# Kernel tuning notes

Hardware: AMD Instinct MI355X
Metric: run time of the kernel (lower is better)

## Reference

```python
import jax, jax.numpy as jnp
import numpy as np

N_NODES = 16384
FM = 256
N_EDGES = 524288


def gcn_conv(x, W, b, edge_index, edge_weight):
    """PyG GCNConv: y = D^-1/2 (A+I) D^-1/2 (x @ W) + b, with edge weights."""
    n = x.shape[0]
    loop = jnp.arange(n)
    src = jnp.concatenate([edge_index[0], loop])
    dst = jnp.concatenate([edge_index[1], loop])
    w = jnp.concatenate([edge_weight, jnp.ones((n,), edge_weight.dtype)])
    deg = jax.ops.segment_sum(w, dst, num_segments=n)
    dinv = jnp.where(deg > 0, jax.lax.rsqrt(jnp.maximum(deg, 1e-30)), 0.0)
    norm = dinv[src] * w * dinv[dst]            # [E+n]
    h = x @ W                                    # [n, fm]
    msg = h[src] * norm[:, None]                 # [E+n, fm] gather
    return jax.ops.segment_sum(msg, dst, num_segments=n) + b


def setup_inputs() -> dict:
    key = jax.random.key(0)
    ks = jax.random.split(key, 24)
    inp = {
        "x": jax.random.normal(ks[0], (N_NODES, FM), jnp.float32),
        "edges_f": jax.random.randint(ks[1], (2, N_EDGES), 0, N_NODES),
        "ew_f": jax.random.uniform(ks[2], (N_EDGES,), jnp.float32),
        "edges_s": jax.random.randint(ks[3], (2, N_EDGES), 0, N_NODES),
        "ew_s": jax.random.uniform(ks[4], (N_EDGES,), jnp.float32),
        "edges_g": jax.random.randint(ks[5], (2, N_EDGES), 0, N_NODES),
        "ew_g": jax.random.uniform(ks[6], (N_EDGES,), jnp.float32),
    }
    names = ["f1", "f2", "s1", "s2", "g1", "g2"]
    for i, nm in enumerate(names):
        inp["W" + nm] = 0.05 * jax.random.normal(ks[7 + i], (FM, FM), jnp.float32)
        inp["b" + nm] = jnp.zeros((FM,), jnp.float32)
    inp["fc1_w"] = 0.5 * jax.random.normal(ks[13], (30, 6), jnp.float32)
    inp["fc1_b"] = jnp.zeros((30,), jnp.float32)
    inp["fc2_w"] = 0.5 * jax.random.normal(ks[14], (6, 30), jnp.float32)
    inp["fc2_b"] = jnp.zeros((6,), jnp.float32)
    inp["cnn_w"] = 0.5 * jax.random.normal(ks[15], (6,), jnp.float32)
    inp["cnn_b"] = jnp.zeros((1,), jnp.float32)
    return inp


def reference(x, edges_f, ew_f, edges_s, ew_s, edges_g, ew_g,
              Wf1, bf1, Wf2, bf2, Ws1, bs1, Ws2, bs2, Wg1, bg1, Wg2, bg2,
              fc1_w, fc1_b, fc2_w, fc2_b, cnn_w, cnn_b):
    # three 2-layer GCN branches with relu
    f1 = jax.nn.relu(gcn_conv(x, Wf1, bf1, edges_f, ew_f))
    f2 = jax.nn.relu(gcn_conv(f1, Wf2, bf2, edges_f, ew_f))
    s1 = jax.nn.relu(gcn_conv(x, Ws1, bs1, edges_s, ew_s))
    s2 = jax.nn.relu(gcn_conv(s1, Ws2, bs2, edges_s, ew_s))
    g1 = jax.nn.relu(gcn_conv(x, Wg1, bg1, edges_g, ew_g))
    g2 = jax.nn.relu(gcn_conv(g1, Wg2, bg2, edges_g, ew_g))
    # cat along features then t().view(1,6,fm,N) == stack of transposed branches
    XM = jnp.stack([f1.T, f2.T, s1.T, s2.T, g1.T, g2.T])  # [6, fm, N]
    # SE channel attention
    pooled = jnp.mean(XM, axis=(1, 2))                     # [6]
    h = jax.nn.relu(fc1_w @ pooled + fc1_b)                # [30]
    att = jax.nn.sigmoid(fc2_w @ h + fc2_b)                # [6]
    XM_att = jax.nn.relu(att[:, None, None] * XM)          # [6, fm, N]
    # 1x1 conv 6->1 channels
    out = jnp.einsum('c,cfn->fn', cnn_w, XM_att) + cnn_b[0]  # [fm, N]
    return out.T                                            # [N, fm]
```

## Files before the change

kernel.cpp:

```cpp
#include <hip/hip_runtime.h>
#include <hip/hip_bf16.h>

#define N_NODES 16384
#define FM      256
#define NF      (N_NODES * FM)
#define NF4     (NF / 4)

typedef __attribute__((ext_vector_type(8))) short short8;
typedef __attribute__((ext_vector_type(4))) float f32x4;

__device__ inline ushort f2bf(float f) {
    uint u = __float_as_uint(f);
    return (ushort)((u + 0x7FFFu + ((u >> 16) & 1u)) >> 16);
}
__device__ inline uint pack2bf(float a, float b) {
    return (uint)f2bf(a) | ((uint)f2bf(b) << 16);
}
__device__ inline float bf2f(ushort u) { return __uint_as_float(((uint)u) << 16); }

__global__ void init_kernel(float* __restrict__ dinv3, int* __restrict__ cnt3,
                            float* __restrict__ pooled) {
    int i = blockIdx.x * blockDim.x + threadIdx.x;
    int n3 = 3 * N_NODES;
    if (i < n3) {
        dinv3[i] = 1.0f;
        cnt3[i] = 0;
    } else if (i < n3 + 6) {
        pooled[i - n3] = 0.0f;
    }
}

__global__ void deg_edges_all(const int* __restrict__ d0, const int* __restrict__ d1,
                              const int* __restrict__ d2,
                              const float* __restrict__ e0, const float* __restrict__ e1,
                              const float* __restrict__ e2,
                              float* __restrict__ deg3, int* __restrict__ cnt3, int E) {
    int t = blockIdx.y;
    const int* dst = (t == 0) ? d0 : (t == 1) ? d1 : d2;
    const float* ew = (t == 0) ? e0 : (t == 1) ? e1 : e2;
    float* deg = deg3 + t * N_NODES;
    int* cnt = cnt3 + t * N_NODES;
    int e = blockIdx.x * blockDim.x + threadIdx.x;
    if (e < E) {
        int d = dst[e];
        atomicAdd(&deg[d], ew[e]);
        atomicAdd(&cnt[d], 1);
    }
}

__global__ void deg_finish_kernel(float* __restrict__ deg, int n3) {
    int i = blockIdx.x * blockDim.x + threadIdx.x;
    if (i < n3) deg[i] = rsqrtf(deg[i]);
}

__global__ __launch_bounds__(1024) void scan_all(const int* __restrict__ cnt3,
                                                 int* __restrict__ rowstart3,
                                                 int* __restrict__ cursor3) {
    const int* cnt = cnt3 + blockIdx.x * N_NODES;
    int* row_start = rowstart3 + blockIdx.x * (N_NODES + 2);
    int* cursor = cursor3 + blockIdx.x * N_NODES;
    __shared__ int part[1024];
    int t = threadIdx.x;
    int base = t * 16;
    int local[16];
    int s = 0;
#pragma unroll
    for (int i = 0; i < 16; ++i) { local[i] = cnt[base + i]; s += local[i]; }
    part[t] = s;
    __syncthreads();
    for (int off = 1; off < 1024; off <<= 1) {
        int v = (t >= off) ? part[t - off] : 0;
        __syncthreads();
        part[t] += v;
        __syncthreads();
    }
    int pre = (t > 0) ? part[t - 1] : 0;
#pragma unroll
    for (int i = 0; i < 16; ++i) {
        row_start[base + i] = pre;
        cursor[base + i] = pre;
        pre += local[i];
    }
    if (t == 1023) row_start[N_NODES] = pre;
}

__global__ void scatter_all(const int* __restrict__ s0, const int* __restrict__ s1,
                            const int* __restrict__ s2,
                            const float* __restrict__ e0, const float* __restrict__ e1,
                            const float* __restrict__ e2,
                            const float* __restrict__ dinv3,
                            int* __restrict__ cursor3,
                            int* __restrict__ csrsrc3, float* __restrict__ csrnorm3,
                            int E) {
    int t = blockIdx.y;
    const int* ed = (t == 0) ? s0 : (t == 1) ? s1 : s2;
    const float* ew = (t == 0) ? e0 : (t == 1) ? e1 : e2;
    const float* dinv = dinv3 + t * N_NODES;
    int* cursor = cursor3 + t * N_NODES;
    int* csr_src = csrsrc3 + (size_t)t * E;
    float* csr_norm = csrnorm3 + (size_t)t * E;
    int e = blockIdx.x * blockDim.x + threadIdx.x;
    if (e >= E) return;
    int s = ed[e], d = ed[E + e];
    int pos = atomicAdd(&cursor[d], 1);
    csr_src[pos] = s;
    csr_norm[pos] = dinv[s] * ew[e] * dinv[d];
}

__global__ __launch_bounds__(256) void wpack_kernel(const float* __restrict__ w0,
                                                    const float* __restrict__ w1,
                                                    const float* __restrict__ w2,
                                                    const float* __restrict__ w3,
                                                    const float* __restrict__ w4,
                                                    const float* __restrict__ w5,
                                                    ushort* __restrict__ wt) {
    const float* W;
    switch (blockIdx.z) {
        case 0: W = w0; break; case 1: W = w1; break; case 2: W = w2; break;
        case 3: W = w3; break; case 4: W = w4; break; default: W = w5; break;
    }
    __shared__ float tl[16][17];
    int tx = threadIdx.x & 15, ty = threadIdx.x >> 4;
    int k0 = blockIdx.x * 16, n0 = blockIdx.y * 16;
    tl[ty][tx] = W[(size_t)(k0 + ty) * FM + n0 + tx];
    __syncthreads();
    wt[(size_t)blockIdx.z * FM * FM + (size_t)(n0 + ty) * FM + k0 + tx] = f2bf(tl[tx][ty]);
}

__global__ __launch_bounds__(256) void gemm_mfma(const float* __restrict__ A,
                                                 const ushort* __restrict__ WT,
                                                 ushort* __restrict__ C) {
    __shared__ ushort A_lds[128 * 64];

    const int tid = threadIdx.x;
    const int lane = tid & 63;
    const int wid = tid >> 6;
    const int wm = wid >> 1, wn = wid & 1;
    const int bm = blockIdx.x * 128;
    const int bn = blockIdx.y * 64;

    const int l15 = lane & 15;
    const int lg = lane >> 4;

    f32x4 acc[4][2];
#pragma unroll
    for (int i = 0; i < 4; ++i)
#pragma unroll
        for (int n = 0; n < 2; ++n) acc[i][n] = (f32x4){0.f, 0.f, 0.f, 0.f};

    const int srow = tid >> 1;
    const int shk = tid & 1;
    const float* arow_p = &A[(size_t)(bm + srow) * FM + shk * 32];

    for (int k0 = 0; k0 < 256; k0 += 64) {
        {
            const float* ap = arow_p + k0;
#pragma unroll
            for (int g = 0; g < 4; ++g) {
                float4 a0 = *(const float4*)(ap + g * 8);
                float4 a1 = *(const float4*)(ap + g * 8 + 4);
                uint4 pk;
                pk.x = pack2bf(a0.x, a0.y);
                pk.y = pack2bf(a0.z, a0.w);
                pk.z = pack2bf(a1.x, a1.y);
                pk.w = pack2bf(a1.z, a1.w);
                int kk = shk * 32 + g * 8;
                int idx = srow * 64 + (kk ^ ((srow & 7) << 3));
                *(uint4*)&A_lds[idx] = pk;
            }
        }
        __syncthreads();
#pragma unroll
        for (int s = 0; s < 2; ++s) {
            short8 bfrag[2];
#pragma unroll
            for (int n = 0; n < 2; ++n) {
                int col = bn + wn * 32 + n * 16 + l15;
                bfrag[n] = *(const short8*)&WT[(size_t)col * FM + k0 + s * 32 + lg * 8];
            }
#pragma unroll
            for (int i = 0; i < 4; ++i) {
                int row = wm * 64 + i * 16 + l15;
                int kk = s * 32 + lg * 8;
                short8 afrag = *(const short8*)&A_lds[row * 64 + (kk ^ ((row & 7) << 3))];
#pragma unroll
                for (int n = 0; n < 2; ++n)
                    acc[i][n] = __builtin_amdgcn_mfma_f32_16x16x32_bf16(
                        afrag, bfrag[n], acc[i][n], 0, 0, 0);
            }
        }
        __syncthreads();
    }
#pragma unroll
    for (int i = 0; i < 4; ++i) {
#pragma unroll
        for (int n = 0; n < 2; ++n) {
            int col = bn + wn * 32 + n * 16 + l15;
#pragma unroll
            for (int r = 0; r < 4; ++r) {
                int row = bm + wm * 64 + i * 16 + lg * 4 + r;
                C[(size_t)row * FM + col] = f2bf(acc[i][n][r]);
            }
        }
    }
}

__global__ __launch_bounds__(256) void gcn_aggregate_csr(const ushort* __restrict__ h,
                                                         const int* __restrict__ row_start,
                                                         const int* __restrict__ csr_src,
                                                         const float* __restrict__ csr_norm,
                                                         const float* __restrict__ dinv,
                                                         const float* __restrict__ bias,
                                                         float* __restrict__ out) {
    int node = blockIdx.x * 4 + (threadIdx.x >> 6);
    int lane = threadIdx.x & 63;
    const ushort4* hp = (const ushort4*)h;

    float di = dinv[node];
    float sw = di * di;
    ushort4 q = hp[(size_t)node * 64 + lane];
    float4 accA = make_float4(bf2f(q.x) * sw, bf2f(q.y) * sw,
                              bf2f(q.z) * sw, bf2f(q.w) * sw);
    float4 accB = make_float4(0.f, 0.f, 0.f, 0.f);

    int beg = row_start[node];
    int end = row_start[node + 1];
    int j = beg;
    for (; j + 3 < end; j += 4) {
        int s0 = csr_src[j];
        int s1 = csr_src[j + 1];
        int s2 = csr_src[j + 2];
        int s3 = csr_src[j + 3];
        float w0 = csr_norm[j];
        float w1 = csr_norm[j + 1];
        float w2 = csr_norm[j + 2];
        float w3 = csr_norm[j + 3];
        ushort4 q0 = hp[(size_t)s0 * 64 + lane];
        ushort4 q1 = hp[(size_t)s1 * 64 + lane];
        ushort4 q2 = hp[(size_t)s2 * 64 + lane];
        ushort4 q3 = hp[(size_t)s3 * 64 + lane];
        accA.x += w0 * bf2f(q0.x) + w1 * bf2f(q1.x);
        accA.y += w0 * bf2f(q0.y) + w1 * bf2f(q1.y);
        accA.z += w0 * bf2f(q0.z) + w1 * bf2f(q1.z);
        accA.w += w0 * bf2f(q0.w) + w1 * bf2f(q1.w);
        accB.x += w2 * bf2f(q2.x) + w3 * bf2f(q3.x);
        accB.y += w2 * bf2f(q2.y) + w3 * bf2f(q3.y);
        accB.z += w2 * bf2f(q2.z) + w3 * bf2f(q3.z);
        accB.w += w2 * bf2f(q2.w) + w3 * bf2f(q3.w);
    }
    for (; j < end; ++j) {
        int s0 = csr_src[j];
        float w0 = csr_norm[j];
        ushort4 q0 = hp[(size_t)s0 * 64 + lane];
        accA.x += w0 * bf2f(q0.x);
        accA.y += w0 * bf2f(q0.y);
        accA.z += w0 * bf2f(q0.z);
        accA.w += w0 * bf2f(q0.w);
    }
    float4 bb = ((const float4*)bias)[lane];
    float4 acc;
    acc.x = fmaxf(accA.x + accB.x + bb.x, 0.0f);
    acc.y = fmaxf(accA.y + accB.y + bb.y, 0.0f);
    acc.z = fmaxf(accA.z + accB.z + bb.z, 0.0f);
    acc.w = fmaxf(accA.w + accB.w + bb.w, 0.0f);
    ((float4*)out)[(size_t)node * 64 + lane] = acc;
}

__global__ __launch_bounds__(256) void reduce_branch_kernel(const float* __restrict__ br,
                                                            float* __restrict__ pooled) {
    int c = blockIdx.y;
    const float4* p = (const float4*)(br + (size_t)c * NF + (size_t)blockIdx.x * 16384);
    float s = 0.0f;
#pragma unroll
    for (int i = 0; i < 16; ++i) {
        float4 v = p[threadIdx.x + i * 256];
        s += v.x + v.y + v.z + v.w;
    }
    for (int o = 32; o > 0; o >>= 1) s += __shfl_down(s, o);
    __shared__ float wsum[4];
    if ((threadIdx.x & 63) == 0) wsum[threadIdx.x >> 6] = s;
    __syncthreads();
    if (threadIdx.x == 0)
        atomicAdd(&pooled[c], wsum[0] + wsum[1] + wsum[2] + wsum[3]);
}

__global__ void se_kernel(const float* __restrict__ pooled_sum,
                          const float* __restrict__ fc1_w, const float* __restrict__ fc1_b,
                          const float* __restrict__ fc2_w, const float* __restrict__ fc2_b,
                          float* __restrict__ att) {
    __shared__ float p[6];
    __shared__ float hbuf[30];
    int t = threadIdx.x;
    if (t < 6) p[t] = pooled_sum[t] * (1.0f / ((float)N_NODES * (float)FM));
    __syncthreads();
    if (t < 30) {
        float a = fc1_b[t];
#pragma unroll
        for (int c = 0; c < 6; ++c) a += fc1_w[t * 6 + c] * p[c];
        hbuf[t] = fmaxf(a, 0.0f);
    }
    __syncthreads();
    if (t < 6) {
        float a = fc2_b[t];
#pragma unroll
        for (int j = 0; j < 30; ++j) a += fc2_w[t * 30 + j] * hbuf[j];
        att[t] = 1.0f / (1.0f + expf(-a));
    }
}

__global__ void combine_kernel(const float* __restrict__ br,
                               const float* __restrict__ att,
                               const float* __restrict__ cnn_w,
                               const float* __restrict__ cnn_b,
                               float* __restrict__ out, int total4) {
    int i = blockIdx.x * blockDim.x + threadIdx.x;
    if (i >= total4) return;
    float a[6], w[6];
#pragma unroll
    for (int c = 0; c < 6; ++c) { a[c] = att[c]; w[c] = cnn_w[c]; }
    float cb = cnn_b[0];
    float4 acc = make_float4(cb, cb, cb, cb);
#pragma unroll
    for (int c = 0; c < 6; ++c) {
        float4 v = ((const float4*)(br + (size_t)c * NF))[i];
        acc.x += w[c] * fmaxf(a[c] * v.x, 0.0f);
        acc.y += w[c] * fmaxf(a[c] * v.y, 0.0f);
        acc.z += w[c] * fmaxf(a[c] * v.z, 0.0f);
        acc.w += w[c] * fmaxf(a[c] * v.w, 0.0f);
    }
    ((float4*)out)[i] = acc;
}


static void run_conv(const float* in, const ushort* wtp, const float* b,
                     const int* row_start, const int* csr_src, const float* csr_norm,
                     const float* dinv, ushort* h_bf16, float* out,
                     hipStream_t stream) {
    dim3 ggrid(N_NODES / 128, FM / 64);
    gemm_mfma<<<ggrid, 256, 0, stream>>>(in, wtp, h_bf16);
    gcn_aggregate_csr<<<N_NODES / 4, 256, 0, stream>>>(h_bf16, row_start, csr_src,
                                                       csr_norm, dinv, b, out);
}

extern "C" void kernel_launch(void* const* d_in, const int* in_sizes, int n_in,
                              void* d_out, int out_size, void* d_ws, size_t ws_size,
                              hipStream_t stream) {
    const float* x      = (const float*)d_in[0];
    const int*   ed_f   = (const int*)d_in[1];
    const float* ew_f   = (const float*)d_in[2];
    const int*   ed_s   = (const int*)d_in[3];
    const float* ew_s   = (const float*)d_in[4];
    const int*   ed_g   = (const int*)d_in[5];
    const float* ew_g   = (const float*)d_in[6];
    const float* Wf1 = (const float*)d_in[7];  const float* bf1 = (const float*)d_in[8];
    const float* Wf2 = (const float*)d_in[9];  const float* bf2 = (const float*)d_in[10];
    const float* Ws1 = (const float*)d_in[11]; const float* bs1 = (const float*)d_in[12];
    const float* Ws2 = (const float*)d_in[13]; const float* bs2 = (const float*)d_in[14];
    const float* Wg1 = (const float*)d_in[15]; const float* bg1 = (const float*)d_in[16];
    const float* Wg2 = (const float*)d_in[17]; const float* bg2 = (const float*)d_in[18];
    const float* fc1_w = (const float*)d_in[19]; const float* fc1_b = (const float*)d_in[20];
    const float* fc2_w = (const float*)d_in[21]; const float* fc2_b = (const float*)d_in[22];
    const float* cnn_w = (const float*)d_in[23]; const float* cnn_b = (const float*)d_in[24];

    const int E = in_sizes[1] / 2;

    float* ws = (float*)d_ws;
    float* br = ws;
    float* dinv3  = ws + (size_t)6 * NF;
    float* pooled = dinv3 + 3 * N_NODES;
    float* att    = pooled + 6;
    int*   cnt3      = (int*)(att + 10);
    int*   cursor3   = cnt3 + 3 * N_NODES;
    int*   rowstart3 = cursor3 + 3 * N_NODES;
    int*   csr_src3  = rowstart3 + 3 * (N_NODES + 2);
    float* csr_norm3 = (float*)(csr_src3 + (size_t)3 * E);
    ushort* wt       = (ushort*)(csr_norm3 + (size_t)3 * E);

    float* dinv_set[3] = { dinv3, dinv3 + N_NODES, dinv3 + 2 * N_NODES };
    int*   rs_set[3]   = { rowstart3, rowstart3 + (N_NODES + 2),
                           rowstart3 + 2 * (N_NODES + 2) };
    int*   csrc_set[3] = { csr_src3, csr_src3 + E, csr_src3 + 2 * E };
    float* cnorm_set[3] = { csr_norm3, csr_norm3 + E, csr_norm3 + 2 * E };

    float* f1 = br + (size_t)0 * NF;
    float* f2 = br + (size_t)1 * NF;
    float* s1 = br + (size_t)2 * NF;
    float* s2 = br + (size_t)3 * NF;
    float* g1 = br + (size_t)4 * NF;
    float* g2 = br + (size_t)5 * NF;

    ushort* h = (ushort*)d_out;

    int n3 = 3 * N_NODES;
    init_kernel<<<(n3 + 6 + 255) / 256, 256, 0, stream>>>(dinv3, cnt3, pooled);
    {
        dim3 dg((E + 255) / 256, 3);
        deg_edges_all<<<dg, 256, 0, stream>>>(ed_f + E, ed_s + E, ed_g + E,
                                              ew_f, ew_s, ew_g, dinv3, cnt3, E);
    }
    deg_finish_kernel<<<(n3 + 255) / 256, 256, 0, stream>>>(dinv3, n3);
    scan_all<<<3, 1024, 0, stream>>>(cnt3, rowstart3, cursor3);
    {
        dim3 sg((E + 255) / 256, 3);
        scatter_all<<<sg, 256, 0, stream>>>(ed_f, ed_s, ed_g, ew_f, ew_s, ew_g,
                                            dinv3, cursor3, csr_src3, csr_norm3, E);
    }
    {
        dim3 wg(16, 16, 6);
        wpack_kernel<<<wg, 256, 0, stream>>>(Wf1, Wf2, Ws1, Ws2, Wg1, Wg2, wt);
    }
    const ushort* wt_set[6] = { wt, wt + 65536, wt + 2 * 65536,
                                wt + 3 * 65536, wt + 4 * 65536, wt + 5 * 65536 };

    run_conv(x,  wt_set[0], bf1, rs_set[0], csrc_set[0], cnorm_set[0], dinv_set[0], h, f1, stream);
    run_conv(f1, wt_set[1], bf2, rs_set[0], csrc_set[0], cnorm_set[0], dinv_set[0], h, f2, stream);
    run_conv(x,  wt_set[2], bs1, rs_set[1], csrc_set[1], cnorm_set[1], dinv_set[1], h, s1, stream);
    run_conv(s1, wt_set[3], bs2, rs_set[1], csrc_set[1], cnorm_set[1], dinv_set[1], h, s2, stream);
    run_conv(x,  wt_set[4], bg1, rs_set[2], csrc_set[2], cnorm_set[2], dinv_set[2], h, g1, stream);
    run_conv(g1, wt_set[5], bg2, rs_set[2], csrc_set[2], cnorm_set[2], dinv_set[2], h, g2, stream);

    dim3 rgrid(256, 6);
    reduce_branch_kernel<<<rgrid, 256, 0, stream>>>(br, pooled);
    se_kernel<<<1, 64, 0, stream>>>(pooled, fc1_w, fc1_b, fc2_w, fc2_b, att);

    combine_kernel<<<NF4 / 256, 256, 0, stream>>>(br, att, cnn_w, cnn_b,
                                                  (float*)d_out, NF4);
}
```

Baseline: 608.5 us.

## Store branch activations in bf16, pack CSR as int2, fuse pooling into aggregation

Branch outputs are now stored as bf16 instead of fp32, which halves the bytes written by aggregation and read by the next GEMM and the combine kernel. x is converted to bf16 once so the GEMM loads bf16 directly. The CSR source index and weight are packed into one int2 array, and degree and norm are computed per row from the CSR instead of with float atomics. The SE mean is accumulated inside the aggregation kernel, which removes the separate reduce pass. The trade-off is extra rounding of intermediate activations and two extra small preprocessing kernels.

```diff
diff --git a/kernel.cpp b/kernel.cpp
--- a/kernel.cpp
+++ b/kernel.cpp
@@ -7,6 +7,7 @@
 #define NF4     (NF / 4)
 
 typedef __attribute__((ext_vector_type(8))) short short8;
+typedef __attribute__((ext_vector_type(8))) ushort ushort8;
 typedef __attribute__((ext_vector_type(4))) float f32x4;
 
 __device__ inline ushort f2bf(float f) {
@@ -18,39 +19,21 @@
 }
 __device__ inline float bf2f(ushort u) { return __uint_as_float(((uint)u) << 16); }
 
-__global__ void init_kernel(float* __restrict__ dinv3, int* __restrict__ cnt3,
-                            float* __restrict__ pooled) {
+__global__ void init_kernel(int* __restrict__ cnt3, float* __restrict__ pooled) {
     int i = blockIdx.x * blockDim.x + threadIdx.x;
     int n3 = 3 * N_NODES;
-    if (i < n3) {
-        dinv3[i] = 1.0f;
-        cnt3[i] = 0;
-    } else if (i < n3 + 6) {
-        pooled[i - n3] = 0.0f;
-    }
-}
-
-__global__ void deg_edges_all(const int* __restrict__ d0, const int* __restrict__ d1,
+    if (i < n3) cnt3[i] = 0;
+    else if (i < n3 + 6) pooled[i - n3] = 0.0f;
+}
+
+__global__ void cnt_edges_all(const int* __restrict__ d0, const int* __restrict__ d1,
                               const int* __restrict__ d2,
-                              const float* __restrict__ e0, const float* __restrict__ e1,
-                              const float* __restrict__ e2,
-                              float* __restrict__ deg3, int* __restrict__ cnt3, int E) {
+                              int* __restrict__ cnt3, int E) {
     int t = blockIdx.y;
     const int* dst = (t == 0) ? d0 : (t == 1) ? d1 : d2;
-    const float* ew = (t == 0) ? e0 : (t == 1) ? e1 : e2;
-    float* deg = deg3 + t * N_NODES;
     int* cnt = cnt3 + t * N_NODES;
     int e = blockIdx.x * blockDim.x + threadIdx.x;
-    if (e < E) {
-        int d = dst[e];
-        atomicAdd(&deg[d], ew[e]);
-        atomicAdd(&cnt[d], 1);
-    }
-}
-
-__global__ void deg_finish_kernel(float* __restrict__ deg, int n3) {
-    int i = blockIdx.x * blockDim.x + threadIdx.x;
-    if (i < n3) deg[i] = rsqrtf(deg[i]);
+    if (e < E) atomicAdd(&cnt[dst[e]], 1);
 }
 
 __global__ __launch_bounds__(1024) void scan_all(const int* __restrict__ cnt3,
@@ -88,23 +71,44 @@
                             const int* __restrict__ s2,
                             const float* __restrict__ e0, const float* __restrict__ e1,
                             const float* __restrict__ e2,
-                            const float* __restrict__ dinv3,
-                            int* __restrict__ cursor3,
-                            int* __restrict__ csrsrc3, float* __restrict__ csrnorm3,
-                            int E) {
+                            int* __restrict__ cursor3, int2* __restrict__ csr3, int E) {
     int t = blockIdx.y;
     const int* ed = (t == 0) ? s0 : (t == 1) ? s1 : s2;
     const float* ew = (t == 0) ? e0 : (t == 1) ? e1 : e2;
-    const float* dinv = dinv3 + t * N_NODES;
     int* cursor = cursor3 + t * N_NODES;
-    int* csr_src = csrsrc3 + (size_t)t * E;
-    float* csr_norm = csrnorm3 + (size_t)t * E;
+    int2* csr = csr3 + (size_t)t * E;
     int e = blockIdx.x * blockDim.x + threadIdx.x;
     if (e >= E) return;
     int s = ed[e], d = ed[E + e];
     int pos = atomicAdd(&cursor[d], 1);
-    csr_src[pos] = s;
-    csr_norm[pos] = dinv[s] * ew[e] * dinv[d];
+    csr[pos] = make_int2(s, __float_as_int(ew[e]));
+}
+
+__global__ __launch_bounds__(256) void deg_dinv_all(const int2* __restrict__ csr3,
+                                                    const int* __restrict__ rowstart3,
+                                                    float* __restrict__ dinv3, int E) {
+    int t = blockIdx.y;
+    const int2* csr = csr3 + (size_t)t * E;
+    const int* row_start = rowstart3 + t * (N_NODES + 2);
+    int node = blockIdx.x * 4 + (threadIdx.x >> 6);
+    int lane = threadIdx.x & 63;
+    int beg = row_start[node], end = row_start[node + 1];
+    float s = 0.0f;
+    for (int j = beg + lane; j < end; j += 64)
+        s += __int_as_float(csr[j].y);
+    for (int o = 32; o > 0; o >>= 1) s += __shfl_down(s, o);
+    if (lane == 0) dinv3[t * N_NODES + node] = rsqrtf(1.0f + s);
+}
+
+__global__ void norm_all(int2* __restrict__ csr3, const float* __restrict__ dinv3,
+                         int E) {
+    int t = blockIdx.y;
+    int2* csr = csr3 + (size_t)t * E;
+    const float* dinv = dinv3 + t * N_NODES;
+    int j = blockIdx.x * blockDim.x + threadIdx.x;
+    if (j >= E) return;
+    int2 c = csr[j];
+    csr[j].y = __float_as_int(__int_as_float(c.y) * dinv[c.x]);
 }
 
 __global__ __launch_bounds__(256) void wpack_kernel(const float* __restrict__ w0,
@@ -127,7 +131,20 @@
     wt[(size_t)blockIdx.z * FM * FM + (size_t)(n0 + ty) * FM + k0 + tx] = f2bf(tl[tx][ty]);
 }
 
-__global__ __launch_bounds__(256) void gemm_mfma(const float* __restrict__ A,
+__global__ void x2bf_kernel(const float* __restrict__ x, ushort* __restrict__ xb) {
+    int i = blockIdx.x * blockDim.x + threadIdx.x;
+    if (i >= NF / 8) return;
+    const float4* xp = (const float4*)x;
+    float4 a = xp[2 * i], b = xp[2 * i + 1];
+    uint4 pk;
+    pk.x = pack2bf(a.x, a.y);
+    pk.y = pack2bf(a.z, a.w);
+    pk.z = pack2bf(b.x, b.y);
+    pk.w = pack2bf(b.z, b.w);
+    ((uint4*)xb)[i] = pk;
+}
+
+__global__ __launch_bounds__(256) void gemm_mfma(const ushort* __restrict__ A,
                                                  const ushort* __restrict__ WT,
                                                  ushort* __restrict__ C) {
     __shared__ ushort A_lds[128 * 64];
@@ -138,7 +155,6 @@
     const int wm = wid >> 1, wn = wid & 1;
     const int bm = blockIdx.x * 128;
     const int bn = blockIdx.y * 64;
-
     const int l15 = lane & 15;
     const int lg = lane >> 4;
 
@@ -150,23 +166,17 @@
 
     const int srow = tid >> 1;
     const int shk = tid & 1;
-    const float* arow_p = &A[(size_t)(bm + srow) * FM + shk * 32];
+    const ushort* arow_p = &A[(size_t)(bm + srow) * FM + shk * 32];
 
     for (int k0 = 0; k0 < 256; k0 += 64) {
         {
-            const float* ap = arow_p + k0;
+            const ushort* ap = arow_p + k0;
 #pragma unroll
             for (int g = 0; g < 4; ++g) {
-                float4 a0 = *(const float4*)(ap + g * 8);
-                float4 a1 = *(const float4*)(ap + g * 8 + 4);
-                uint4 pk;
-                pk.x = pack2bf(a0.x, a0.y);
-                pk.y = pack2bf(a0.z, a0.w);
-                pk.z = pack2bf(a1.x, a1.y);
-                pk.w = pack2bf(a1.z, a1.w);
+                ushort8 v = *(const ushort8*)(ap + g * 8);
                 int kk = shk * 32 + g * 8;
                 int idx = srow * 64 + (kk ^ ((srow & 7) << 3));
-                *(uint4*)&A_lds[idx] = pk;
+                *(ushort8*)&A_lds[idx] = v;
             }
         }
         __syncthreads();
@@ -207,38 +217,36 @@
 
 __global__ __launch_bounds__(256) void gcn_aggregate_csr(const ushort* __restrict__ h,
                                                          const int* __restrict__ row_start,
-                                                         const int* __restrict__ csr_src,
-                                                         const float* __restrict__ csr_norm,
+                                                         const int2* __restrict__ csr,
                                                          const float* __restrict__ dinv,
                                                          const float* __restrict__ bias,
-                                                         float* __restrict__ out) {
+                                                         ushort* __restrict__ out,
+                                                         float* __restrict__ pooled,
+                                                         int bidx) {
     int node = blockIdx.x * 4 + (threadIdx.x >> 6);
     int lane = threadIdx.x & 63;
     const ushort4* hp = (const ushort4*)h;
 
-    float di = dinv[node];
-    float sw = di * di;
     ushort4 q = hp[(size_t)node * 64 + lane];
-    float4 accA = make_float4(bf2f(q.x) * sw, bf2f(q.y) * sw,
-                              bf2f(q.z) * sw, bf2f(q.w) * sw);
+    float4 accA = make_float4(0.f, 0.f, 0.f, 0.f);
     float4 accB = make_float4(0.f, 0.f, 0.f, 0.f);
 
     int beg = row_start[node];
     int end = row_start[node + 1];
     int j = beg;
     for (; j + 3 < end; j += 4) {
-        int s0 = csr_src[j];
-        int s1 = csr_src[j + 1];
-        int s2 = csr_src[j + 2];
-        int s3 = csr_src[j + 3];
-        float w0 = csr_norm[j];
-        float w1 = csr_norm[j + 1];
-        float w2 = csr_norm[j + 2];
-        float w3 = csr_norm[j + 3];
-        ushort4 q0 = hp[(size_t)s0 * 64 + lane];
-        ushort4 q1 = hp[(size_t)s1 * 64 + lane];
-        ushort4 q2 = hp[(size_t)s2 * 64 + lane];
-        ushort4 q3 = hp[(size_t)s3 * 64 + lane];
+        int2 c0 = csr[j];
+        int2 c1 = csr[j + 1];
+        int2 c2 = csr[j + 2];
+        int2 c3 = csr[j + 3];
+        float w0 = __int_as_float(c0.y);
+        float w1 = __int_as_float(c1.y);
+        float w2 = __int_as_float(c2.y);
+        float w3 = __int_as_float(c3.y);
+        ushort4 q0 = hp[(size_t)c0.x * 64 + lane];
+        ushort4 q1 = hp[(size_t)c1.x * 64 + lane];
+        ushort4 q2 = hp[(size_t)c2.x * 64 + lane];
+        ushort4 q3 = hp[(size_t)c3.x * 64 + lane];
         accA.x += w0 * bf2f(q0.x) + w1 * bf2f(q1.x);
         accA.y += w0 * bf2f(q0.y) + w1 * bf2f(q1.y);
         accA.z += w0 * bf2f(q0.z) + w1 * bf2f(q1.z);
@@ -249,39 +257,32 @@
         accB.w += w2 * bf2f(q2.w) + w3 * bf2f(q3.w);
     }
     for (; j < end; ++j) {
-        int s0 = csr_src[j];
-        float w0 = csr_norm[j];
-        ushort4 q0 = hp[(size_t)s0 * 64 + lane];
+        int2 c0 = csr[j];
+        float w0 = __int_as_float(c0.y);
+        ushort4 q0 = hp[(size_t)c0.x * 64 + lane];
         accA.x += w0 * bf2f(q0.x);
         accA.y += w0 * bf2f(q0.y);
         accA.z += w0 * bf2f(q0.z);
         accA.w += w0 * bf2f(q0.w);
     }
+    float di = dinv[node];
     float4 bb = ((const float4*)bias)[lane];
-    float4 acc;
-    acc.x = fmaxf(accA.x + accB.x + bb.x, 0.0f);
-    acc.y = fmaxf(accA.y + accB.y + bb.y, 0.0f);
-    acc.z = fmaxf(accA.z + accB.z + bb.z, 0.0f);
-    acc.w = fmaxf(accA.w + accB.w + bb.w, 0.0f);
-    ((float4*)out)[(size_t)node * 64 + lane] = acc;
-}
-
-__global__ __launch_bounds__(256) void reduce_branch_kernel(const float* __restrict__ br,
-                                                            float* __restrict__ pooled) {
-    int c = blockIdx.y;
-    const float4* p = (const float4*)(br + (size_t)c * NF + (size_t)blockIdx.x * 16384);
-    float s = 0.0f;
-#pragma unroll
-    for (int i = 0; i < 16; ++i) {
-        float4 v = p[threadIdx.x + i * 256];
-        s += v.x + v.y + v.z + v.w;
-    }
-    for (int o = 32; o > 0; o >>= 1) s += __shfl_down(s, o);
+    float4 r;
+    r.x = fmaxf(di * (di * bf2f(q.x) + accA.x + accB.x) + bb.x, 0.0f);
+    r.y = fmaxf(di * (di * bf2f(q.y) + accA.y + accB.y) + bb.y, 0.0f);
+    r.z = fmaxf(di * (di * bf2f(q.z) + accA.z + accB.z) + bb.z, 0.0f);
+    r.w = fmaxf(di * (di * bf2f(q.w) + accA.w + accB.w) + bb.w, 0.0f);
+    ushort4 o;
+    o.x = f2bf(r.x); o.y = f2bf(r.y); o.z = f2bf(r.z); o.w = f2bf(r.w);
+    ((ushort4*)out)[(size_t)node * 64 + lane] = o;
+
+    float psum = r.x + r.y + r.z + r.w;
+    for (int o2 = 32; o2 > 0; o2 >>= 1) psum += __shfl_down(psum, o2);
     __shared__ float wsum[4];
-    if ((threadIdx.x & 63) == 0) wsum[threadIdx.x >> 6] = s;
+    if (lane == 0) wsum[threadIdx.x >> 6] = psum;
     __syncthreads();
     if (threadIdx.x == 0)
-        atomicAdd(&pooled[c], wsum[0] + wsum[1] + wsum[2] + wsum[3]);
+        atomicAdd(&pooled[bidx], wsum[0] + wsum[1] + wsum[2] + wsum[3]);
 }
 
 __global__ void se_kernel(const float* __restrict__ pooled_sum,
@@ -308,7 +309,7 @@
     }
 }
 
-__global__ void combine_kernel(const float* __restrict__ br,
+__global__ void combine_kernel(const ushort* __restrict__ br,
                                const float* __restrict__ att,
                                const float* __restrict__ cnn_w,
                                const float* __restrict__ cnn_b,
@@ -322,24 +323,24 @@
     float4 acc = make_float4(cb, cb, cb, cb);
 #pragma unroll
     for (int c = 0; c < 6; ++c) {
-        float4 v = ((const float4*)(br + (size_t)c * NF))[i];
-        acc.x += w[c] * fmaxf(a[c] * v.x, 0.0f);
-        acc.y += w[c] * fmaxf(a[c] * v.y, 0.0f);
-        acc.z += w[c] * fmaxf(a[c] * v.z, 0.0f);
-        acc.w += w[c] * fmaxf(a[c] * v.w, 0.0f);
+        ushort4 q = ((const ushort4*)(br + (size_t)c * NF))[i];
+        acc.x += w[c] * fmaxf(a[c] * bf2f(q.x), 0.0f);
+        acc.y += w[c] * fmaxf(a[c] * bf2f(q.y), 0.0f);
+        acc.z += w[c] * fmaxf(a[c] * bf2f(q.z), 0.0f);
+        acc.w += w[c] * fmaxf(a[c] * bf2f(q.w), 0.0f);
     }
     ((float4*)out)[i] = acc;
 }
 
 
-static void run_conv(const float* in, const ushort* wtp, const float* b,
-                     const int* row_start, const int* csr_src, const float* csr_norm,
-                     const float* dinv, ushort* h_bf16, float* out,
+static void run_conv(const ushort* inA, const ushort* wtp, const float* b,
+                     const int* row_start, const int2* csr, const float* dinv,
+                     ushort* h_bf16, ushort* out, float* pooled, int bidx,
                      hipStream_t stream) {
     dim3 ggrid(N_NODES / 128, FM / 64);
-    gemm_mfma<<<ggrid, 256, 0, stream>>>(in, wtp, h_bf16);
-    gcn_aggregate_csr<<<N_NODES / 4, 256, 0, stream>>>(h_bf16, row_start, csr_src,
-                                                       csr_norm, dinv, b, out);
+    gemm_mfma<<<ggrid, 256, 0, stream>>>(inA, wtp, h_bf16);
+    gcn_aggregate_csr<<<N_NODES / 4, 256, 0, stream>>>(h_bf16, row_start, csr,
+                                                       dinv, b, out, pooled, bidx);
 }
 
 extern "C" void kernel_launch(void* const* d_in, const int* in_sizes, int n_in,
@@ -364,65 +365,69 @@
 
     const int E = in_sizes[1] / 2;
 
-    float* ws = (float*)d_ws;
-    float* br = ws;
-    float* dinv3  = ws + (size_t)6 * NF;
-    float* pooled = dinv3 + 3 * N_NODES;
-    float* att    = pooled + 6;
-    int*   cnt3      = (int*)(att + 10);
-    int*   cursor3   = cnt3 + 3 * N_NODES;
-    int*   rowstart3 = cursor3 + 3 * N_NODES;
-    int*   csr_src3  = rowstart3 + 3 * (N_NODES + 2);
-    float* csr_norm3 = (float*)(csr_src3 + (size_t)3 * E);
-    ushort* wt       = (ushort*)(csr_norm3 + (size_t)3 * E);
+    ushort* br_u  = (ushort*)d_ws;
+    ushort* xb    = br_u + (size_t)6 * NF;
+    ushort* wt    = xb + NF;
+    float*  dinv3 = (float*)(wt + 6 * FM * FM);
+    float*  pooled = dinv3 + 3 * N_NODES;
+    float*  att    = pooled + 8;
+    int*    cnt3      = (int*)(att + 8);
+    int*    cursor3   = cnt3 + 3 * N_NODES;
+    int*    rowstart3 = cursor3 + 3 * N_NODES;
+    int2*   csr3      = (int2*)(rowstart3 + 3 * (N_NODES + 2) + 2);
 
     float* dinv_set[3] = { dinv3, dinv3 + N_NODES, dinv3 + 2 * N_NODES };
     int*   rs_set[3]   = { rowstart3, rowstart3 + (N_NODES + 2),
                            rowstart3 + 2 * (N_NODES + 2) };
-    int*   csrc_set[3] = { csr_src3, csr_src3 + E, csr_src3 + 2 * E };
-    float* cnorm_set[3] = { csr_norm3, csr_norm3 + E, csr_norm3 + 2 * E };
-
-    float* f1 = br + (size_t)0 * NF;
-    float* f2 = br + (size_t)1 * NF;
-    float* s1 = br + (size_t)2 * NF;
-    float* s2 = br + (size_t)3 * NF;
-    float* g1 = br + (size_t)4 * NF;
-    float* g2 = br + (size_t)5 * NF;
+    int2*  csr_set[3]  = { csr3, csr3 + E, csr3 + 2 * E };
+
+    ushort* f1 = br_u + (size_t)0 * NF;
+    ushort* f2 = br_u + (size_t)1 * NF;
+    ushort* s1 = br_u + (size_t)2 * NF;
+    ushort* s2 = br_u + (size_t)3 * NF;
+    ushort* g1 = br_u + (size_t)4 * NF;
+    ushort* g2 = br_u + (size_t)5 * NF;
 
     ushort* h = (ushort*)d_out;
 
     int n3 = 3 * N_NODES;
-    init_kernel<<<(n3 + 6 + 255) / 256, 256, 0, stream>>>(dinv3, cnt3, pooled);
+    init_kernel<<<(n3 + 6 + 255) / 256, 256, 0, stream>>>(cnt3, pooled);
     {
-        dim3 dg((E + 255) / 256, 3);
-        deg_edges_all<<<dg, 256, 0, stream>>>(ed_f + E, ed_s + E, ed_g + E,
-                                              ew_f, ew_s, ew_g, dinv3, cnt3, E);
-    }
-    deg_finish_kernel<<<(n3 + 255) / 256, 256, 0, stream>>>(dinv3, n3);
+        dim3 g((E + 255) / 256, 3);
+        cnt_edges_all<<<g, 256, 0, stream>>>(ed_f + E, ed_s + E, ed_g + E, cnt3, E);
+    }
     scan_all<<<3, 1024, 0, stream>>>(cnt3, rowstart3, cursor3);
     {
-        dim3 sg((E + 255) / 256, 3);
-        scatter_all<<<sg, 256, 0, stream>>>(ed_f, ed_s, ed_g, ew_f, ew_s, ew_g,
-                                            dinv3, cursor3, csr_src3, csr_norm3, E);
+        dim3 g((E + 255) / 256, 3);
+        scatter_all<<<g, 256, 0, stream>>>(ed_f, ed_s, ed_g, ew_f, ew_s, ew_g,
+                                           cursor3, csr3, E);
+    }
+    {
+        dim3 g(N_NODES / 4, 3);
+        deg_dinv_all<<<g, 256, 0, stream>>>(csr3, rowstart3, dinv3, E);
+    }
+    {
+        dim3 g((E + 255) / 256, 3);
+        norm_all<<<g, 256, 0, stream>>>(csr3, dinv3, E);
     }
     {
         dim3 wg(16, 16, 6);
         wpack_kernel<<<wg, 256, 0, stream>>>(Wf1, Wf2, Ws1, Ws2, Wg1, Wg2, wt);
     }
+    x2bf_kernel<<<(NF / 8 + 255) / 256, 256, 0, stream>>>(x, xb);
+
     const ushort* wt_set[6] = { wt, wt + 65536, wt + 2 * 65536,
                                 wt + 3 * 65536, wt + 4 * 65536, wt + 5 * 65536 };
 
-    run_conv(x,  wt_set[0], bf1, rs_set[0], csrc_set[0], cnorm_set[0], dinv_set[0], h, f1, stream);
-    run_conv(f1, wt_set[1], bf2, rs_set[0], csrc_set[0], cnorm_set[0], dinv_set[0], h, f2, stream);
-    run_conv(x,  wt_set[2], bs1, rs_set[1], csrc_set[1], cnorm_set[1], dinv_set[1], h, s1, stream);
-    run_conv(s1, wt_set[3], bs2, rs_set[1], csrc_set[1], cnorm_set[1], dinv_set[1], h, s2, stream);
-    run_conv(x,  wt_set[4], bg1, rs_set[2], csrc_set[2], cnorm_set[2], dinv_set[2], h, g1, stream);
-    run_conv(g1, wt_set[5], bg2, rs_set[2], csrc_set[2], cnorm_set[2], dinv_set[2], h, g2, stream);
-
-    dim3 rgrid(256, 6);
-    reduce_branch_kernel<<<rgrid, 256, 0, stream>>>(br, pooled);
+    run_conv(xb, wt_set[0], bf1, rs_set[0], csr_set[0], dinv_set[0], h, f1, pooled, 0, stream);
+    run_conv(f1, wt_set[1], bf2, rs_set[0], csr_set[0], dinv_set[0], h, f2, pooled, 1, stream);
+    run_conv(xb, wt_set[2], bs1, rs_set[1], csr_set[1], dinv_set[1], h, s1, pooled, 2, stream);
+    run_conv(s1, wt_set[3], bs2, rs_set[1], csr_set[1], dinv_set[1], h, s2, pooled, 3, stream);
+    run_conv(xb, wt_set[4], bg1, rs_set[2], csr_set[2], dinv_set[2], h, g1, pooled, 4, stream);
+    run_conv(g1, wt_set[5], bg2, rs_set[2], csr_set[2], dinv_set[2], h, g2, pooled, 5, stream);
+
     se_kernel<<<1, 64, 0, stream>>>(pooled, fc1_w, fc1_b, fc2_w, fc2_b, att);
 
-    combine_kernel<<<NF4 / 256, 256, 0, stream>>>(br, att, cnn_w, cnn_b,
+    combine_kernel<<<NF4 / 256, 256, 0, stream>>>(br_u, att, cnn_w, cnn_b,
                                                   (float*)d_out, NF4);
 }
```

Measured after the change: 704.5 us. +15.8%, slower.
